# Kernel optimization log

Measured on AMD Instinct MI355X. Metric: run time of the kernel, lower is better.

## Reference

```python
import jax, jax.numpy as jnp
import numpy as np

B, T, C, HS = 4, 4096, 1024, 64


def setup_inputs() -> dict:
    key = jax.random.key(0)
    kx, kq, kk, kv = jax.random.split(key, 4)
    x = jax.random.normal(kx, (B, T, C), dtype=jnp.float32)
    s = 1.0 / np.sqrt(C)
    Wq = jax.random.normal(kq, (C, HS), dtype=jnp.float32) * s
    Wk = jax.random.normal(kk, (C, HS), dtype=jnp.float32) * s
    Wv = jax.random.normal(kv, (C, HS), dtype=jnp.float32) * s
    return {"x": x, "Wq": Wq, "Wk": Wk, "Wv": Wv}


def reference(x, Wq, Wk, Wv):
    # q,k,v: [B, T, HS]
    q = x @ Wq
    k = x @ Wk
    v = x @ Wv
    scale = k.shape[-1] ** -0.5
    # full T x T causal attention scores, as the torch module materializes
    scores = jnp.einsum('bqh,bkh->bqk', q, k) * scale  # [B, T, T]
    t = x.shape[1]
    causal = jnp.tril(jnp.ones((t, t), dtype=bool))
    scores = jnp.where(causal[None, :, :], scores, -jnp.inf)
    wei = jax.nn.softmax(scores, axis=-1)  # dropout = 0.0 (eval)
    out = jnp.einsum('bqk,bkh->bqh', wei, v)  # [B, T, HS]
    return out
```

## Files before the change

kernel.cpp:

```cpp
#include <hip/hip_runtime.h>
#include <math.h>

#define BB 4
#define TT 4096
#define CC 1024
#define HS 64
#define MM (BB*TT)

typedef __attribute__((ext_vector_type(8))) short short8;
typedef __attribute__((ext_vector_type(4))) float f32x4;
typedef __attribute__((ext_vector_type(4))) unsigned short ushort4v;

__device__ __forceinline__ unsigned short f2bf(float f) {
    union { float f; unsigned u; } v; v.f = f;
    return (unsigned short)((v.u + 0x7fffu + ((v.u >> 16) & 1u)) >> 16);
}

__global__ __launch_bounds__(256) void prep_kernel(
    const float* __restrict__ Wq, const float* __restrict__ Wk,
    const float* __restrict__ Wv, unsigned short* __restrict__ Wt)
{
    const int which = blockIdx.x >> 4;
    const int k0 = (blockIdx.x & 15) * 64;
    const float* __restrict__ W = (which == 0) ? Wq : (which == 1) ? Wk : Wv;
    const float scale = (which == 0) ? 0.125f : 1.0f;
    __shared__ unsigned short lds[64][65];
    const int t = threadIdx.x;
    #pragma unroll
    for (int i = 0; i < 16; i++) {
        int idx = t + 256 * i;
        int r = idx >> 6, n = idx & 63;
        lds[r][n] = f2bf(W[(size_t)(k0 + r) * 64 + n] * scale);
    }
    __syncthreads();
    #pragma unroll
    for (int i = 0; i < 16; i++) {
        int idx = t + 256 * i;
        int n = idx >> 6, r = idx & 63;
        Wt[(which << 16) + (n << 10) + k0 + r] = lds[r][n];
    }
}

__global__ __launch_bounds__(256, 2) void qkv_mfma(
    const float* __restrict__ x, const unsigned short* __restrict__ Wt,
    unsigned short* __restrict__ qb, unsigned short* __restrict__ kb,
    unsigned short* __restrict__ vT)
{
    const int rt = blockIdx.x;
    __shared__ unsigned short xs[32][136];
    __shared__ unsigned short ws[192][136];

    const int t = threadIdx.x;
    const int w = t >> 6;
    const int lane = t & 63;
    const int quad = lane >> 4;
    const int c = lane & 15;

    float4 xreg[4];
    short8 wreg[12];
    #pragma unroll
    for (int i = 0; i < 4; i++) {
        int idx = t + 256 * i;
        int r = idx >> 5, c4 = (idx & 31) * 4;
        xreg[i] = *(const float4*)(x + (size_t)(rt * 32 + r) * CC + c4);
    }
    #pragma unroll
    for (int i = 0; i < 12; i++) {
        int idx = t + 256 * i;
        int n = idx >> 4, c8 = (idx & 15) * 8;
        wreg[i] = *(const short8*)(Wt + (size_t)n * CC + c8);
    }

    f32x4 acc[2][3];
    #pragma unroll
    for (int mt = 0; mt < 2; mt++)
        #pragma unroll
        for (int j = 0; j < 3; j++) acc[mt][j] = (f32x4){0.f, 0.f, 0.f, 0.f};

    for (int k0 = 0; k0 < CC; k0 += 128) {
        __syncthreads();
        #pragma unroll
        for (int i = 0; i < 4; i++) {
            int idx = t + 256 * i;
            int r = idx >> 5, c4 = (idx & 31) * 4;
            ushort4v p = { f2bf(xreg[i].x), f2bf(xreg[i].y), f2bf(xreg[i].z), f2bf(xreg[i].w) };
            *(ushort4v*)&xs[r][c4] = p;
        }
        #pragma unroll
        for (int i = 0; i < 12; i++) {
            int idx = t + 256 * i;
            int n = idx >> 4, c8 = (idx & 15) * 8;
            *(short8*)&ws[n][c8] = wreg[i];
        }
        if (k0 + 128 < CC) {
            #pragma unroll
            for (int i = 0; i < 4; i++) {
                int idx = t + 256 * i;
                int r = idx >> 5, c4 = (idx & 31) * 4;
                xreg[i] = *(const float4*)(x + (size_t)(rt * 32 + r) * CC + k0 + 128 + c4);
            }
            #pragma unroll
            for (int i = 0; i < 12; i++) {
                int idx = t + 256 * i;
                int n = idx >> 4, c8 = (idx & 15) * 8;
                wreg[i] = *(const short8*)(Wt + (size_t)n * CC + k0 + 128 + c8);
            }
        }
        __syncthreads();
        #pragma unroll
        for (int ks = 0; ks < 4; ks++) {
            short8 af[2], bf[3];
            #pragma unroll
            for (int mt = 0; mt < 2; mt++)
                af[mt] = *(const short8*)&xs[16 * mt + c][ks * 32 + quad * 8];
            #pragma unroll
            for (int j = 0; j < 3; j++)
                bf[j] = *(const short8*)&ws[16 * (w + 4 * j) + c][ks * 32 + quad * 8];
            #pragma unroll
            for (int mt = 0; mt < 2; mt++)
                #pragma unroll
                for (int j = 0; j < 3; j++)
                    acc[mt][j] = __builtin_amdgcn_mfma_f32_16x16x32_bf16(af[mt], bf[j], acc[mt][j], 0, 0, 0);
        }
    }

    __syncthreads();
    unsigned short (*vtb)[72] = (unsigned short (*)[72])ws;
    #pragma unroll
    for (int mt = 0; mt < 2; mt++) {
        int grow = rt * 32 + 16 * mt + quad * 4;
        #pragma unroll
        for (int reg = 0; reg < 4; reg++) {
            qb[(size_t)(grow + reg) * HS + 16 * w + c] = f2bf(acc[mt][0][reg]);
            kb[(size_t)(grow + reg) * HS + 16 * w + c] = f2bf(acc[mt][1][reg]);
            vtb[16 * w + c][16 * mt + quad * 4 + reg] = f2bf(acc[mt][2][reg]);
        }
    }
    __syncthreads();
    {
        const int b  = rt >> 7;
        const int t0 = (rt & 127) * 32;
        int d = t >> 2, c8 = (t & 3) * 8;
        short8 v0 = *(const short8*)&vtb[d][c8];
        *(short8*)(vT + (size_t)b * HS * TT + (size_t)d * TT + t0 + c8) = v0;
    }
}

__global__ __launch_bounds__(256, 4) void attn_mfma(
    const unsigned short* __restrict__ qb, const unsigned short* __restrict__ kb,
    const unsigned short* __restrict__ vT, float* __restrict__ Opart,
    float* __restrict__ lpart)
{
    const int bid = blockIdx.x;
    const int qt = (TT / 64 - 1) - (bid >> 4);
    const int j  = (bid >> 2) & 3;
    const int b  = bid & 3;

    __shared__ unsigned short ks[64][72];
    __shared__ unsigned short vt[64][72];
    __shared__ unsigned short ps[4][16][72];

    const int t = threadIdx.x;
    const int w = t >> 6;
    const int lane = t & 63;
    const int quad = lane >> 4;
    const int c = lane & 15;
    const int qrow = qt * 64 + 16 * w;

    short8 aq[2];
    #pragma unroll
    for (int kstep = 0; kstep < 2; kstep++)
        aq[kstep] = *(const short8*)(qb + (size_t)(b * TT + qrow + c) * HS + kstep * 32 + quad * 8);

    const int nkt = (qt >= j) ? ((qt - j) >> 2) + 1 : 0;
    const unsigned short* Kb = kb + (size_t)b * TT * HS;
    const unsigned short* Vb = vT + (size_t)b * HS * TT;

    const int srow = t >> 3;
    const int sc8  = (t & 7) * 8;

    short8 kreg[2], vreg[2];
    if (nkt > 0) {
        const int kt0 = j * 64;
        #pragma unroll
        for (int i = 0; i < 2; i++) {
            kreg[i] = *(const short8*)(Kb + (size_t)(kt0 + srow + 32 * i) * HS + sc8);
            vreg[i] = *(const short8*)(Vb + (size_t)(srow + 32 * i) * TT + kt0 + sc8);
        }
    }

    float l[4] = {0.f, 0.f, 0.f, 0.f};
    f32x4 oacc[4];
    #pragma unroll
    for (int dt = 0; dt < 4; dt++) oacc[dt] = (f32x4){0.f, 0.f, 0.f, 0.f};

    for (int i = 0; i < nkt; i++) {
        const int kt = j + 4 * i;
        const int kt0 = kt * 64;
        __syncthreads();
        #pragma unroll
        for (int ii = 0; ii < 2; ii++) {
            *(short8*)&ks[srow + 32 * ii][sc8] = kreg[ii];
            *(short8*)&vt[srow + 32 * ii][sc8] = vreg[ii];
        }
        if (i + 1 < nkt) {
            const int nb = kt0 + 256;
            #pragma unroll
            for (int ii = 0; ii < 2; ii++) {
                kreg[ii] = *(const short8*)(Kb + (size_t)(nb + srow + 32 * ii) * HS + sc8);
                vreg[ii] = *(const short8*)(Vb + (size_t)(srow + 32 * ii) * TT + nb + sc8);
            }
        }
        __syncthreads();

        f32x4 sc[4];
        #pragma unroll
        for (int st = 0; st < 4; st++) sc[st] = (f32x4){0.f, 0.f, 0.f, 0.f};
        #pragma unroll
        for (int kstep = 0; kstep < 2; kstep++) {
            #pragma unroll
            for (int st = 0; st < 4; st++) {
                short8 bf = *(const short8*)&ks[16 * st + c][kstep * 32 + quad * 8];
                sc[st] = __builtin_amdgcn_mfma_f32_16x16x32_bf16(aq[kstep], bf, sc[st], 0, 0, 0);
            }
        }
        if (kt == qt) {
            #pragma unroll
            for (int st = 0; st < 4; st++)
                #pragma unroll
                for (int reg = 0; reg < 4; reg++) {
                    int kg = kt0 + 16 * st + c;
                    int qg = qrow + quad * 4 + reg;
                    float p = (kg <= qg) ? __expf(sc[st][reg]) : 0.f;
                    sc[st][reg] = p;
                    l[reg] += p;
                }
        } else {
            #pragma unroll
            for (int st = 0; st < 4; st++)
                #pragma unroll
                for (int reg = 0; reg < 4; reg++) {
                    float p = __expf(sc[st][reg]);
                    sc[st][reg] = p;
                    l[reg] += p;
                }
        }
        #pragma unroll
        for (int st = 0; st < 4; st++)
            #pragma unroll
            for (int reg = 0; reg < 4; reg++)
                ps[w][quad * 4 + reg][16 * st + c] = f2bf(sc[st][reg]);

        #pragma unroll
        for (int kstep = 0; kstep < 2; kstep++) {
            short8 ap = *(const short8*)&ps[w][c][kstep * 32 + quad * 8];
            #pragma unroll
            for (int dt = 0; dt < 4; dt++) {
                short8 bv = *(const short8*)&vt[16 * dt + c][kstep * 32 + quad * 8];
                oacc[dt] = __builtin_amdgcn_mfma_f32_16x16x32_bf16(ap, bv, oacc[dt], 0, 0, 0);
            }
        }
    }

    #pragma unroll
    for (int reg = 0; reg < 4; reg++)
        #pragma unroll
        for (int msk = 1; msk < 16; msk <<= 1)
            l[reg] += __shfl_xor(l[reg], msk);

    float* __restrict__ Oj = Opart + (size_t)j * MM * HS;
    #pragma unroll
    for (int dt = 0; dt < 4; dt++)
        #pragma unroll
        for (int reg = 0; reg < 4; reg++)
            Oj[(size_t)(b * TT + qrow + quad * 4 + reg) * HS + 16 * dt + c] = oacc[dt][reg];
    if (c == 0)
        #pragma unroll
        for (int reg = 0; reg < 4; reg++)
            lpart[(size_t)j * MM + b * TT + qrow + quad * 4 + reg] = l[reg];
}

__global__ __launch_bounds__(256) void combine_kernel(
    const float* __restrict__ Opart, const float* __restrict__ lpart,
    float* __restrict__ out)
{
    const int id = blockIdx.x * 256 + threadIdx.x;
    const int row = id >> 4;
    float l = lpart[row] + lpart[MM + row] + lpart[2 * MM + row] + lpart[3 * MM + row];
    const float4* O = (const float4*)Opart;
    const size_t stride = (size_t)MM * HS / 4;
    float4 a = O[id], b = O[id + stride], c = O[id + 2 * stride], d = O[id + 3 * stride];
    float inv = 1.f / l;
    float4 r;
    r.x = (a.x + b.x + c.x + d.x) * inv;
    r.y = (a.y + b.y + c.y + d.y) * inv;
    r.z = (a.z + b.z + c.z + d.z) * inv;
    r.w = (a.w + b.w + c.w + d.w) * inv;
    ((float4*)out)[id] = r;
}

extern "C" void kernel_launch(void* const* d_in, const int* in_sizes, int n_in,
                              void* d_out, int out_size, void* d_ws, size_t ws_size,
                              hipStream_t stream) {
    const float* x  = (const float*)d_in[0];
    const float* Wq = (const float*)d_in[1];
    const float* Wk = (const float*)d_in[2];
    const float* Wv = (const float*)d_in[3];
    float* out = (float*)d_out;

    unsigned short* Wt   = (unsigned short*)d_ws;
    unsigned short* qbuf = Wt + 3 * 64 * 1024;
    unsigned short* kbuf = qbuf + (size_t)MM * HS;
    unsigned short* vTb  = kbuf + (size_t)MM * HS;
    float* Opart = (float*)(vTb + (size_t)MM * HS);
    float* lpart = Opart + 4 * (size_t)MM * HS;

    prep_kernel<<<48, 256, 0, stream>>>(Wq, Wk, Wv, Wt);
    qkv_mfma<<<MM / 32, 256, 0, stream>>>(x, Wt, qbuf, kbuf, vTb);
    attn_mfma<<<BB * (TT / 64) * 4, 256, 0, stream>>>(qbuf, kbuf, vTb, Opart, lpart);
    combine_kernel<<<1024, 256, 0, stream>>>(Opart, lpart, out);
}
```

Measured before the change: 136.8 us.

## Double-buffer QKV projection with direct-register weights and tune attention loop scheduling

The QKV projection kernel now loads weight MFMA fragments straight from global memory into registers instead of staging them through LDS. It double-buffers the x tile in LDS, with a fully unrolled software pipeline that issues loads one chunk ahead, which drops LDS traffic and one barrier per chunk. The attention loop moves its barrier before the next-tile prefetch, raises wave priority around the MFMA blocks with s_setprio, and packs bf16 conversions using v_cvt_pk_bf16_f32. The costs are higher register pressure from 24 short8 weight fragments and less coalesced weight loads.

Measured after the change: 145.2 us. 6.2% more time.

```diff
diff --git a/kernel.cpp b/kernel.cpp
--- a/kernel.cpp
+++ b/kernel.cpp
@@ -14,6 +14,12 @@
 __device__ __forceinline__ unsigned short f2bf(float f) {
     union { float f; unsigned u; } v; v.f = f;
     return (unsigned short)((v.u + 0x7fffu + ((v.u >> 16) & 1u)) >> 16);
+}
+
+__device__ __forceinline__ unsigned cvt_pk_bf16(float lo, float hi) {
+    unsigned r;
+    asm("v_cvt_pk_bf16_f32 %0, %1, %2" : "=v"(r) : "v"(lo), "v"(hi));
+    return r;
 }
 
 __global__ __launch_bounds__(256) void prep_kernel(
@@ -47,8 +53,8 @@
     unsigned short* __restrict__ vT)
 {
     const int rt = blockIdx.x;
-    __shared__ unsigned short xs[32][136];
-    __shared__ unsigned short ws[192][136];
+    __shared__ unsigned short xs[2][32][136];
+    __shared__ unsigned short vtb[64][72];
 
     const int t = threadIdx.x;
     const int w = t >> 6;
@@ -56,20 +62,49 @@
     const int quad = lane >> 4;
     const int c = lane & 15;
 
+    const int xrow = t >> 5;
+    const int xcol = (t & 31) * 4;
+    const float* __restrict__ xp = x + (size_t)(rt * 32 + xrow) * CC + xcol;
+
+    const unsigned short* __restrict__ wp0 = Wt + (size_t)(16 * (w + 0) + c) * CC + quad * 8;
+    const unsigned short* __restrict__ wp1 = Wt + (size_t)(16 * (w + 4) + c) * CC + quad * 8;
+    const unsigned short* __restrict__ wp2 = Wt + (size_t)(16 * (w + 8) + c) * CC + quad * 8;
+
     float4 xreg[4];
-    short8 wreg[12];
-    #pragma unroll
-    for (int i = 0; i < 4; i++) {
-        int idx = t + 256 * i;
-        int r = idx >> 5, c4 = (idx & 31) * 4;
-        xreg[i] = *(const float4*)(x + (size_t)(rt * 32 + r) * CC + c4);
-    }
-    #pragma unroll
-    for (int i = 0; i < 12; i++) {
-        int idx = t + 256 * i;
-        int n = idx >> 4, c8 = (idx & 15) * 8;
-        wreg[i] = *(const short8*)(Wt + (size_t)n * CC + c8);
-    }
+    short8 wfa[12], wfb[12];
+
+#define LOAD_X(CK) do { \
+    _Pragma("unroll") \
+    for (int i_ = 0; i_ < 4; i_++) \
+        xreg[i_] = *(const float4*)(xp + (size_t)(8 * i_) * CC + (CK) * 128); \
+    } while (0)
+
+#define STAGE_X(BUF) do { \
+    _Pragma("unroll") \
+    for (int i_ = 0; i_ < 4; i_++) { \
+        ushort4v p_ = { f2bf(xreg[i_].x), f2bf(xreg[i_].y), \
+                        f2bf(xreg[i_].z), f2bf(xreg[i_].w) }; \
+        *(ushort4v*)&xs[BUF][xrow + 8 * i_][xcol] = p_; \
+    } } while (0)
+
+#define LOAD_W(DST, CK) do { \
+    _Pragma("unroll") \
+    for (int s_ = 0; s_ < 4; s_++) { \
+        DST[s_ * 3 + 0] = *(const short8*)(wp0 + (CK) * 128 + s_ * 32); \
+        DST[s_ * 3 + 1] = *(const short8*)(wp1 + (CK) * 128 + s_ * 32); \
+        DST[s_ * 3 + 2] = *(const short8*)(wp2 + (CK) * 128 + s_ * 32); \
+    } } while (0)
+
+#define COMPUTE(BUF, WF) do { \
+    _Pragma("unroll") \
+    for (int s_ = 0; s_ < 4; s_++) { \
+        short8 af0_ = *(const short8*)&xs[BUF][c][s_ * 32 + quad * 8]; \
+        short8 af1_ = *(const short8*)&xs[BUF][16 + c][s_ * 32 + quad * 8]; \
+        _Pragma("unroll") \
+        for (int j_ = 0; j_ < 3; j_++) { \
+            acc[0][j_] = __builtin_amdgcn_mfma_f32_16x16x32_bf16(af0_, WF[s_ * 3 + j_], acc[0][j_], 0, 0, 0); \
+            acc[1][j_] = __builtin_amdgcn_mfma_f32_16x16x32_bf16(af1_, WF[s_ * 3 + j_], acc[1][j_], 0, 0, 0); \
+        } } } while (0)
 
     f32x4 acc[2][3];
     #pragma unroll
@@ -77,55 +112,25 @@
         #pragma unroll
         for (int j = 0; j < 3; j++) acc[mt][j] = (f32x4){0.f, 0.f, 0.f, 0.f};
 
-    for (int k0 = 0; k0 < CC; k0 += 128) {
-        __syncthreads();
-        #pragma unroll
-        for (int i = 0; i < 4; i++) {
-            int idx = t + 256 * i;
-            int r = idx >> 5, c4 = (idx & 31) * 4;
-            ushort4v p = { f2bf(xreg[i].x), f2bf(xreg[i].y), f2bf(xreg[i].z), f2bf(xreg[i].w) };
-            *(ushort4v*)&xs[r][c4] = p;
-        }
-        #pragma unroll
-        for (int i = 0; i < 12; i++) {
-            int idx = t + 256 * i;
-            int n = idx >> 4, c8 = (idx & 15) * 8;
-            *(short8*)&ws[n][c8] = wreg[i];
-        }
-        if (k0 + 128 < CC) {
-            #pragma unroll
-            for (int i = 0; i < 4; i++) {
-                int idx = t + 256 * i;
-                int r = idx >> 5, c4 = (idx & 31) * 4;
-                xreg[i] = *(const float4*)(x + (size_t)(rt * 32 + r) * CC + k0 + 128 + c4);
-            }
-            #pragma unroll
-            for (int i = 0; i < 12; i++) {
-                int idx = t + 256 * i;
-                int n = idx >> 4, c8 = (idx & 15) * 8;
-                wreg[i] = *(const short8*)(Wt + (size_t)n * CC + k0 + 128 + c8);
-            }
-        }
-        __syncthreads();
-        #pragma unroll
-        for (int ks = 0; ks < 4; ks++) {
-            short8 af[2], bf[3];
-            #pragma unroll
-            for (int mt = 0; mt < 2; mt++)
-                af[mt] = *(const short8*)&xs[16 * mt + c][ks * 32 + quad * 8];
-            #pragma unroll
-            for (int j = 0; j < 3; j++)
-                bf[j] = *(const short8*)&ws[16 * (w + 4 * j) + c][ks * 32 + quad * 8];
-            #pragma unroll
-            for (int mt = 0; mt < 2; mt++)
-                #pragma unroll
-                for (int j = 0; j < 3; j++)
-                    acc[mt][j] = __builtin_amdgcn_mfma_f32_16x16x32_bf16(af[mt], bf[j], acc[mt][j], 0, 0, 0);
-        }
-    }
-
-    __syncthreads();
-    unsigned short (*vtb)[72] = (unsigned short (*)[72])ws;
+    LOAD_X(0);
+    LOAD_W(wfa, 0);
+    STAGE_X(0);
+    LOAD_X(1);
+
+    __syncthreads(); LOAD_W(wfb, 1); STAGE_X(1); LOAD_X(2); COMPUTE(0, wfa);
+    __syncthreads(); LOAD_W(wfa, 2); STAGE_X(0); LOAD_X(3); COMPUTE(1, wfb);
+    __syncthreads(); LOAD_W(wfb, 3); STAGE_X(1); LOAD_X(4); COMPUTE(0, wfa);
+    __syncthreads(); LOAD_W(wfa, 4); STAGE_X(0); LOAD_X(5); COMPUTE(1, wfb);
+    __syncthreads(); LOAD_W(wfb, 5); STAGE_X(1); LOAD_X(6); COMPUTE(0, wfa);
+    __syncthreads(); LOAD_W(wfa, 6); STAGE_X(0); LOAD_X(7); COMPUTE(1, wfb);
+    __syncthreads(); LOAD_W(wfb, 7); STAGE_X(1);            COMPUTE(0, wfa);
+    __syncthreads();                                        COMPUTE(1, wfb);
+
+#undef LOAD_X
+#undef STAGE_X
+#undef LOAD_W
+#undef COMPUTE
+
     #pragma unroll
     for (int mt = 0; mt < 2; mt++) {
         int grow = rt * 32 + 16 * mt + quad * 4;
@@ -203,6 +208,8 @@
             *(short8*)&ks[srow + 32 * ii][sc8] = kreg[ii];
             *(short8*)&vt[srow + 32 * ii][sc8] = vreg[ii];
         }
+        __syncthreads();
+
         if (i + 1 < nkt) {
             const int nb = kt0 + 256;
             #pragma unroll
@@ -211,11 +218,11 @@
                 vreg[ii] = *(const short8*)(Vb + (size_t)(srow + 32 * ii) * TT + nb + sc8);
             }
         }
-        __syncthreads();
 
         f32x4 sc[4];
         #pragma unroll
         for (int st = 0; st < 4; st++) sc[st] = (f32x4){0.f, 0.f, 0.f, 0.f};
+        __builtin_amdgcn_s_setprio(1);
         #pragma unroll
         for (int kstep = 0; kstep < 2; kstep++) {
             #pragma unroll
@@ -224,6 +231,7 @@
                 sc[st] = __builtin_amdgcn_mfma_f32_16x16x32_bf16(aq[kstep], bf, sc[st], 0, 0, 0);
             }
         }
+        __builtin_amdgcn_s_setprio(0);
         if (kt == qt) {
             #pragma unroll
             for (int st = 0; st < 4; st++)
@@ -246,11 +254,16 @@
                 }
         }
         #pragma unroll
-        for (int st = 0; st < 4; st++)
-            #pragma unroll
-            for (int reg = 0; reg < 4; reg++)
-                ps[w][quad * 4 + reg][16 * st + c] = f2bf(sc[st][reg]);
-
+        for (int st = 0; st < 4; st++) {
+            unsigned p01 = cvt_pk_bf16(sc[st][0], sc[st][1]);
+            unsigned p23 = cvt_pk_bf16(sc[st][2], sc[st][3]);
+            ps[w][quad * 4 + 0][16 * st + c] = (unsigned short)p01;
+            ps[w][quad * 4 + 1][16 * st + c] = (unsigned short)(p01 >> 16);
+            ps[w][quad * 4 + 2][16 * st + c] = (unsigned short)p23;
+            ps[w][quad * 4 + 3][16 * st + c] = (unsigned short)(p23 >> 16);
+        }
+
+        __builtin_amdgcn_s_setprio(1);
         #pragma unroll
         for (int kstep = 0; kstep < 2; kstep++) {
             short8 ap = *(const short8*)&ps[w][c][kstep * 32 + quad * 8];
@@ -260,6 +273,7 @@
                 oacc[dt] = __builtin_amdgcn_mfma_f32_16x16x32_bf16(ap, bv, oacc[dt], 0, 0, 0);
             }
         }
+        __builtin_amdgcn_s_setprio(0);
     }
 
     #pragma unroll
```
